# Kernel tuning notes

Measured on AMD Instinct MI355X. Metric: run time of the kernel, lower is better.

The kernel has to match this reference:

```python
import jax, jax.numpy as jnp
import numpy as np

B, L, D = 2, 2048, 2048
H, KV = 32, 8
HD = D // H          # 64
REP = H // KV        # 4


def setup_inputs() -> dict:
    key = jax.random.key(0)
    ks = jax.random.split(key, 6)
    x = jax.random.normal(ks[0], (B, L, D), dtype=jnp.float32)
    # weights stored [in, out] (transpose of torch Linear weight), scaled for stability
    wq = jax.random.normal(ks[1], (D, H * HD), dtype=jnp.float32) * 0.02
    wk = jax.random.normal(ks[2], (D, KV * HD), dtype=jnp.float32) * 0.02
    wv = jax.random.normal(ks[3], (D, KV * HD), dtype=jnp.float32) * 0.02
    wo = jax.random.normal(ks[4], (H * HD, D), dtype=jnp.float32) * 0.02
    # RoPE frequencies: freqs_cis = exp(i * pos * theta), theta_j = 10000^{-2j/HD}
    inv_freq = 1.0 / (10000.0 ** (jnp.arange(0, HD, 2, dtype=jnp.float32) / HD))  # [HD/2]
    angles = jnp.arange(L, dtype=jnp.float32)[:, None] * inv_freq[None, :]        # [L, HD/2]
    freqs_cos = jnp.cos(angles)
    freqs_sin = jnp.sin(angles)
    # additive causal mask [L, L] (prefill from start_pos=0)
    mask = jnp.where(jnp.tril(jnp.ones((L, L), dtype=bool)), 0.0, -jnp.inf).astype(jnp.float32)
    return {"x": x, "start_pos": 0, "freqs_cos": freqs_cos, "freqs_sin": freqs_sin,
            "mask": mask, "wq": wq, "wk": wk, "wv": wv, "wo": wo}


def _apply_rope(t, cos, sin):
    # t: [B, L, h, HD]; cos/sin: [L, HD/2] -> broadcast [1, L, 1, HD/2]
    tp = t.reshape(*t.shape[:-1], HD // 2, 2)
    a, b = tp[..., 0], tp[..., 1]
    c = cos[None, :, None, :]
    s = sin[None, :, None, :]
    ra = a * c - b * s
    rb = a * s + b * c
    return jnp.stack([ra, rb], axis=-1).reshape(t.shape)


def reference(x, start_pos, freqs_cos, freqs_sin, mask, wq, wk, wv, wo):
    xq = jnp.einsum('bld,de->ble', x, wq).reshape(B, L, H, HD)
    xk = jnp.einsum('bld,de->ble', x, wk).reshape(B, L, KV, HD)
    xv = jnp.einsum('bld,de->ble', x, wv).reshape(B, L, KV, HD)
    xq = _apply_rope(xq, freqs_cos, freqs_sin)
    xk = _apply_rope(xk, freqs_cos, freqs_sin)
    # (cache write of xk/xv is a dead side effect in the torch module; omitted)
    # GQA: query head (g*REP + r) attends to kv head g  == repeat_interleave semantics
    q = xq.transpose(0, 2, 1, 3).reshape(B, KV, REP, L, HD)  # [B,KV,REP,L,HD]
    k = xk.transpose(0, 2, 1, 3)                              # [B,KV,L,HD]
    v = xv.transpose(0, 2, 1, 3)
    scale = 1.0 / jnp.sqrt(jnp.float32(HD))
    scores = jnp.einsum('bgrld,bgmd->bgrlm', q, k) * scale + mask  # [B,KV,REP,L,L]
    attn = jax.nn.softmax(scores, axis=-1)
    out = jnp.einsum('bgrlm,bgmd->bgrld', attn, v)            # [B,KV,REP,L,HD]
    out = out.reshape(B, H, L, HD).transpose(0, 2, 1, 3).reshape(B, L, H * HD)
    return jnp.einsum('ble,ed->bld', out, wo)
```

## Files before the change

### kernel.cpp

```cpp
#include <hip/hip_runtime.h>
#include <hip/hip_bf16.h>
#include <math.h>

typedef __bf16 bf16_t;
typedef __bf16 bf16x8 __attribute__((ext_vector_type(8)));
typedef __bf16 bf16x4 __attribute__((ext_vector_type(4)));
typedef __bf16 bf16x2 __attribute__((ext_vector_type(2)));
typedef float  f32x4  __attribute__((ext_vector_type(4)));
typedef int    i32x4  __attribute__((ext_vector_type(4)));

#define B_  2
#define L_  2048
#define D_  2048
#define H_  32
#define KV_ 8
#define HD_ 64

static __device__ __forceinline__ void gload_lds16(const bf16_t* g, void* l)
{
    __builtin_amdgcn_global_load_lds(
        (const __attribute__((address_space(1))) void*)g,
        (__attribute__((address_space(3))) void*)l, 16, 0, 0);
}

static __device__ __forceinline__ int packbf(float a, float b)
{
    bf16x2 t; t[0] = (bf16_t)a; t[1] = (bf16_t)b;
    return __builtin_bit_cast(int, t);
}

static __device__ __forceinline__ void pl32(int& a, int& b)
{
    asm("v_permlane32_swap_b32 %0, %1" : "+v"(a), "+v"(b));
}
static __device__ __forceinline__ void pl16(int& a, int& b)
{
    asm("v_permlane16_swap_b32 %0, %1" : "+v"(a), "+v"(b));
}

#define WAITV8() asm volatile("s_waitcnt vmcnt(8)" ::: "memory")
#define WAITV4() asm volatile("s_waitcnt vmcnt(4)" ::: "memory")
#define WAITV2() asm volatile("s_waitcnt vmcnt(2)" ::: "memory")
#define WAITV0() asm volatile("s_waitcnt vmcnt(0)" ::: "memory")
#define WAITL0() asm volatile("s_waitcnt lgkmcnt(0)" ::: "memory")

__global__ void cast_f32_bf16(const float4* __restrict__ in,
                              bf16x4* __restrict__ out, int n4)
{
    const int i = blockIdx.x * 256 + threadIdx.x;
    if (i >= n4) return;
    const float4 v = in[i];
    bf16x4 o;
    o[0] = (bf16_t)v.x; o[1] = (bf16_t)v.y; o[2] = (bf16_t)v.z; o[3] = (bf16_t)v.w;
    out[i] = o;
}

template <typename InT>
__global__ void transpose_cast(const InT* __restrict__ in, bf16_t* __restrict__ out,
                               int R, int C)
{
    __shared__ bf16_t tile[32][33];
    const int bx = blockIdx.x * 32, by = blockIdx.y * 32;
    in  += (size_t)blockIdx.z * R * C;
    out += (size_t)blockIdx.z * R * C;
    const int tx = threadIdx.x, ty = threadIdx.y;
#pragma unroll
    for (int i = ty; i < 32; i += 8)
        tile[i][tx] = (bf16_t)(float)in[(size_t)(by + i) * C + bx + tx];
    __syncthreads();
#pragma unroll
    for (int i = ty; i < 32; i += 8)
        out[(size_t)(bx + i) * R + by + tx] = tile[tx][i];
}

#define FRAG(base, row, kk) \
    (*(const bf16x8*)((base) + (size_t)(row) * 128 + ((((kk) * 4 + quad) ^ sw8) << 4)))

#define STG_A(kt, h, buf) do {                                                        \
    gload_lds16(Ag + (size_t)((h) * 128)      * 2048 + (size_t)(kt) * 64,             \
                sdst + (buf) * 32768 + (h) * 16384);                                  \
    gload_lds16(Ag + (size_t)((h) * 128 + 64) * 2048 + (size_t)(kt) * 64,             \
                sdst + (buf) * 32768 + (h) * 16384 + 8192);                           \
} while (0)

#define STG_B(kt, h, buf) do {                                                        \
    gload_lds16(Bg + (size_t)((h) * 128)      * 2048 + (size_t)(kt) * 64,             \
                sdst + 65536 + (buf) * 32768 + (h) * 16384);                          \
    gload_lds16(Bg + (size_t)((h) * 128 + 64) * 2048 + (size_t)(kt) * 64,             \
                sdst + 65536 + (buf) * 32768 + (h) * 16384 + 8192);                   \
} while (0)

#define PHASE_SET(AB, BB, STG1, STG2, STG3, STG4, VM4)                                \
  {                                        \
    _Pragma("unroll") for (int m = 0; m < 4; m++) {                                   \
        Afr[m][0] = FRAG(AB, arow + m * 16, 0);                                       \
        Afr[m][1] = FRAG(AB, arow + m * 16, 1); }                                     \
    _Pragma("unroll") for (int n = 0; n < 2; n++) {                                   \
        B01[n][0] = FRAG(BB, brow + n * 16, 0);                                       \
        B01[n][1] = FRAG(BB, brow + n * 16, 1); }                                     \
    STG1;                                                                             \
    asm volatile("s_waitcnt lgkmcnt(8)" ::: "memory");                                \
    __builtin_amdgcn_s_barrier();                                                     \
    WAITL0();                                                                         \
    __builtin_amdgcn_s_setprio(1);                                                    \
    _Pragma("unroll") for (int m = 0; m < 4; m++)                                     \
      _Pragma("unroll") for (int n = 0; n < 2; n++)                                   \
        _Pragma("unroll") for (int kk = 0; kk < 2; kk++)                              \
          acc[m][n] = __builtin_amdgcn_mfma_f32_16x16x32_bf16(                        \
              Afr[m][kk], B01[n][kk], acc[m][n], 0, 0, 0);                            \
    __builtin_amdgcn_s_setprio(0);                                                    \
    __builtin_amdgcn_s_barrier();                                                     \
  }                                                                                   \
  {                                                 \
    _Pragma("unroll") for (int n = 0; n < 2; n++) {                                   \
        B23[n][0] = FRAG(BB, brow + (n + 2) * 16, 0);                                 \
        B23[n][1] = FRAG(BB, brow + (n + 2) * 16, 1); }                               \
    STG2;                                                                             \
    __builtin_amdgcn_s_barrier();                                                     \
    WAITL0();                                                                         \
    __builtin_amdgcn_s_setprio(1);                                                    \
    _Pragma("unroll") for (int m = 0; m < 4; m++)                                     \
      _Pragma("unroll") for (int n = 0; n < 2; n++)                                   \
        _Pragma("unroll") for (int kk = 0; kk < 2; kk++)                              \
          acc[m][n + 2] = __builtin_amdgcn_mfma_f32_16x16x32_bf16(                    \
              Afr[m][kk], B23[n][kk], acc[m][n + 2], 0, 0, 0);                        \
    __builtin_amdgcn_s_setprio(0);                                                    \
    __builtin_amdgcn_s_barrier();                                                     \
  }                                                                                   \
  {                                                 \
    _Pragma("unroll") for (int m = 0; m < 4; m++) {                                   \
        Afr[m][0] = FRAG(AB, arow + (m + 4) * 16, 0);                                 \
        Afr[m][1] = FRAG(AB, arow + (m + 4) * 16, 1); }                               \
    STG3;                                                                             \
    __builtin_amdgcn_s_barrier();                                                     \
    WAITL0();                                                                         \
    __builtin_amdgcn_s_setprio(1);                                                    \
    _Pragma("unroll") for (int m = 0; m < 4; m++)                                     \
      _Pragma("unroll") for (int n = 0; n < 2; n++)                                   \
        _Pragma("unroll") for (int kk = 0; kk < 2; kk++)                              \
          acc[m + 4][n + 2] = __builtin_amdgcn_mfma_f32_16x16x32_bf16(                \
              Afr[m][kk], B23[n][kk], acc[m + 4][n + 2], 0, 0, 0);                    \
    __builtin_amdgcn_s_setprio(0);                                                    \
    __builtin_amdgcn_s_barrier();                                                     \
  }                                                                                   \
  {                                        \
    STG4;                                                                             \
    VM4;                                                                              \
    __builtin_amdgcn_s_barrier();                                                     \
    __builtin_amdgcn_s_setprio(1);                                                    \
    _Pragma("unroll") for (int m = 0; m < 4; m++)                                     \
      _Pragma("unroll") for (int n = 0; n < 2; n++)                                   \
        _Pragma("unroll") for (int kk = 0; kk < 2; kk++)                              \
          acc[m + 4][n] = __builtin_amdgcn_mfma_f32_16x16x32_bf16(                    \
              Afr[m][kk], B01[n][kk], acc[m + 4][n], 0, 0, 0);                        \
    __builtin_amdgcn_s_setprio(0);                                                    \
    __builtin_amdgcn_s_barrier();                                                     \
  }

__global__ __launch_bounds__(512, 2) void gemm_qkv(
    const bf16_t* __restrict__ A,
    const bf16_t* __restrict__ BT,
    bf16_t* __restrict__ Qb, bf16_t* __restrict__ Kb, bf16_t* __restrict__ Vb)
{
    extern __shared__ __attribute__((aligned(16))) char DLDS[];
    constexpr int NITER = 2048 / 64 / 2;

    const int tid  = threadIdx.x;
    const int wave = tid >> 6;
    const int lane = tid & 63;
    const int quad = lane >> 4;
    const int l16  = lane & 15;
    const int wr   = wave >> 2;
    const int wc   = wave & 3;
    const int m0   = blockIdx.y * 256;
    const int n0   = blockIdx.x * 256;

    const int srow  = tid >> 3;
    const int swcol = ((tid & 7) ^ (srow & 7)) * 8;
    const bf16_t* Ag = A  + (size_t)(m0 + srow) * 2048 + swcol;
    const bf16_t* Bg = BT + (size_t)(n0 + srow) * 2048 + swcol;
    char* sdst = DLDS + tid * 16;

    const char* AB0 = DLDS;
    const char* AB1 = DLDS + 32768;
    const char* BB0 = DLDS + 65536;
    const char* BB1 = DLDS + 98304;
    const int sw8  = l16 & 7;
    const int arow = wr * 128 + l16;
    const int brow = wc * 64 + l16;

    f32x4 acc[8][4];
    const f32x4 zf = {0.f, 0.f, 0.f, 0.f};
#pragma unroll
    for (int i = 0; i < 8; i++)
#pragma unroll
        for (int j = 0; j < 4; j++) acc[i][j] = zf;

    bf16x8 Afr[4][2], B01[2][2], B23[2][2];

    STG_B(0, 0, 0); STG_B(0, 1, 0); STG_A(0, 0, 0); STG_A(0, 1, 0);
    STG_B(1, 0, 1); STG_B(1, 1, 1);
    WAITV4();
    __builtin_amdgcn_s_barrier();

    for (int i = 0; i < NITER; ++i) {
        const int t1 = 2 * i + 1;
        const int t2 = 2 * i + 2;
        const int t3 = 2 * i + 3;
        const bool more = (i + 1 < NITER);

        PHASE_SET(AB0, BB0,
                  STG_A(t1, 0, 1),
                  STG_A(t1, 1, 1),
                  if (more) STG_B(t2, 0, 0),
                  if (more) STG_B(t2, 1, 0),
                  if (more) { WAITV4(); } else { WAITV0(); })
        PHASE_SET(AB1, BB1,
                  if (more) STG_A(t2, 0, 0),
                  if (more) STG_A(t2, 1, 0),
                  if (more) STG_B(t3, 0, 1),
                  if (more) STG_B(t3, 1, 1),
                  WAITV4())
    }

    bf16_t* Cb; int ldc, coff; float cs = 1.f;
    if (n0 < 2048)      { Cb = Qb; ldc = 2048; coff = 0; }
    else if (n0 < 2560) { Cb = Kb; ldc = 512;  coff = 2048;
                          cs = 0.18033688011112042f; }
    else                { Cb = Vb; ldc = 512;  coff = 2560; }

#pragma unroll
    for (int mt = 0; mt < 8; mt++)
#pragma unroll
        for (int nt = 0; nt < 4; nt++)
#pragma unroll
            for (int r = 0; r < 4; r++) {
                const int row = m0 + wr * 128 + mt * 16 + quad * 4 + r;
                const int col = n0 + wc * 64 + nt * 16 + l16 - coff;
                Cb[(size_t)row * ldc + col] = (bf16_t)(acc[mt][nt][r] * cs);
            }
}

#undef FRAG
#undef STG_A
#undef STG_B
#undef PHASE_SET

#define OFRAG(base, row, kk) \
    (*(const bf16x8*)((base) + (size_t)(row) * 128 + ((((kk) * 4 + quad) ^ sw8) << 4)))

#define OSTG_A(kt, h, buf) do {                                                       \
    gload_lds16(Ag + (size_t)((h) * 128)      * 2048 + (size_t)(kt) * 64,             \
                adst + (buf) * 32768 + (h) * 16384);                                  \
    gload_lds16(Ag + (size_t)((h) * 128 + 64) * 2048 + (size_t)(kt) * 64,             \
                adst + (buf) * 32768 + (h) * 16384 + 8192);                           \
} while (0)

#define OSTG_B(kt, buf) do {                                                          \
    gload_lds16(Bg + (size_t)(kt) * 64,                       bdst + (buf) * 16384);  \
    gload_lds16(Bg + (size_t)64 * 2048 + (size_t)(kt) * 64,   bdst + (buf) * 16384 + 8192); \
} while (0)

#define OTILE(AB, BB, SA, SB, VMW)                                                    \
  {                                             \
    _Pragma("unroll") for (int m = 0; m < 4; m++) {                                   \
        Afr[m][0] = OFRAG(AB, arow + m * 16, 0);                                      \
        Afr[m][1] = OFRAG(AB, arow + m * 16, 1); }                                    \
    _Pragma("unroll") for (int n = 0; n < 2; n++) {                                   \
        Bfr[n][0] = OFRAG(BB, brow + n * 16, 0);                                      \
        Bfr[n][1] = OFRAG(BB, brow + n * 16, 1); }                                    \
    SA;                                                                               \
    asm volatile("s_waitcnt lgkmcnt(8)" ::: "memory");                                \
    __builtin_amdgcn_s_barrier();                                                     \
    WAITL0();                                                                         \
    __builtin_amdgcn_s_setprio(1);                                                    \
    _Pragma("unroll") for (int m = 0; m < 4; m++)                                     \
      _Pragma("unroll") for (int n = 0; n < 2; n++)                                   \
        _Pragma("unroll") for (int kk = 0; kk < 2; kk++)                              \
          acc[m][n] = __builtin_amdgcn_mfma_f32_16x16x32_bf16(                        \
              Afr[m][kk], Bfr[n][kk], acc[m][n], 0, 0, 0);                            \
    __builtin_amdgcn_s_setprio(0);                                                    \
    __builtin_amdgcn_s_barrier();                                                     \
  }                                                                                   \
  {                                \
    _Pragma("unroll") for (int m = 0; m < 4; m++) {                                   \
        Afr[m][0] = OFRAG(AB, arow + (m + 4) * 16, 0);                                \
        Afr[m][1] = OFRAG(AB, arow + (m + 4) * 16, 1); }                              \
    SB;                                                                               \
    VMW;                                                                              \
    __builtin_amdgcn_s_barrier();                                                     \
    WAITL0();                                                                         \
    __builtin_amdgcn_s_setprio(1);                                                    \
    _Pragma("unroll") for (int m = 0; m < 4; m++)                                     \
      _Pragma("unroll") for (int n = 0; n < 2; n++)                                   \
        _Pragma("unroll") for (int kk = 0; kk < 2; kk++)                              \
          acc[m + 4][n] = __builtin_amdgcn_mfma_f32_16x16x32_bf16(                    \
              Afr[m][kk], Bfr[n][kk], acc[m + 4][n], 0, 0, 0);                        \
    __builtin_amdgcn_s_setprio(0);                                                    \
    __builtin_amdgcn_s_barrier();                                                     \
  }

__global__ __launch_bounds__(512, 2) void gemm_out(
    const bf16_t* __restrict__ A,
    const bf16_t* __restrict__ BT,
    float* __restrict__ C)
{
    extern __shared__ __attribute__((aligned(16))) char DLDS[];
    constexpr int NITER = 2048 / 64 / 2;

    const int tid  = threadIdx.x;
    const int wave = tid >> 6;
    const int lane = tid & 63;
    const int quad = lane >> 4;
    const int l16  = lane & 15;
    const int wr   = wave >> 2;
    const int wc   = wave & 3;

    const int id   = blockIdx.x;
    const int w    = id >> 3;
    const int m0   = ((id & 7) * 2 + (w & 1)) * 256;
    const int n0   = (w >> 1) * 128;

    const int srow  = tid >> 3;
    const int swcol = ((tid & 7) ^ (srow & 7)) * 8;
    const bf16_t* Ag = A  + (size_t)(m0 + srow) * 2048 + swcol;
    const bf16_t* Bg = BT + (size_t)(n0 + srow) * 2048 + swcol;
    char* adst = DLDS + tid * 16;
    char* bdst = DLDS + 65536 + tid * 16;

    const char* AB0 = DLDS;
    const char* AB1 = DLDS + 32768;
    const char* BB0 = DLDS + 65536;
    const char* BB1 = DLDS + 81920;
    const int sw8  = l16 & 7;
    const int arow = wr * 128 + l16;
    const int brow = wc * 32 + l16;

    f32x4 acc[8][2];
    const f32x4 zf = {0.f, 0.f, 0.f, 0.f};
#pragma unroll
    for (int i = 0; i < 8; i++)
#pragma unroll
        for (int j = 0; j < 2; j++) acc[i][j] = zf;

    bf16x8 Afr[4][2], Bfr[2][2];

    OSTG_B(0, 0); OSTG_A(0, 0, 0); OSTG_A(0, 1, 0); OSTG_B(1, 1);
    WAITV2();
    __builtin_amdgcn_s_barrier();

    for (int i = 0; i < NITER; ++i) {
        const int v  = 2 * i + 1;
        const int t2 = 2 * i + 2;
        const int t3 = 2 * i + 3;
        const bool more = (i + 1 < NITER);

        OTILE(AB0, BB0,
              { OSTG_A(v, 0, 1); OSTG_A(v, 1, 1); },
              { if (more) OSTG_B(t2, 0); },
              if (more) { WAITV2(); } else { WAITV0(); })
        OTILE(AB1, BB1,
              { if (more) { OSTG_A(t2, 0, 0); OSTG_A(t2, 1, 0); } },
              { if (more) OSTG_B(t3, 1); },
              if (more) { WAITV2(); } else { WAITV0(); })
    }

#pragma unroll
    for (int mt = 0; mt < 8; mt++)
#pragma unroll
        for (int nt = 0; nt < 2; nt++)
#pragma unroll
            for (int r = 0; r < 4; r++) {
                const int row = m0 + wr * 128 + mt * 16 + quad * 4 + r;
                const int col = n0 + wc * 32 + nt * 16 + l16;
                C[(size_t)row * 2048 + col] = acc[mt][nt][r];
            }
}

#undef OFRAG
#undef OSTG_A
#undef OSTG_B
#undef OTILE

__global__ void rope_k(bf16_t* __restrict__ T, const float* __restrict__ fc,
                       const float* __restrict__ fs, int nheads, int total8)
{
    const int idx = blockIdx.x * 256 + threadIdx.x;
    if (idx >= total8) return;
    const int g  = idx & 7;
    const int t  = idx >> 3;
    const int h  = t % nheads;
    const int bl = t / nheads;
    const int l  = bl & (L_ - 1);
    const float4 c4 = *(const float4*)(fc + l * 32 + g * 4);
    const float4 s4 = *(const float4*)(fs + l * 32 + g * 4);
    const size_t off = ((size_t)bl * nheads + h) * 64 + g * 8;
    const bf16x8 v = *(const bf16x8*)(T + off);
    const float cc[4] = {c4.x, c4.y, c4.z, c4.w};
    const float ss[4] = {s4.x, s4.y, s4.z, s4.w};
    bf16x8 o;
#pragma unroll
    for (int p = 0; p < 4; p++) {
        const float a  = (float)v[2 * p];
        const float b2 = (float)v[2 * p + 1];
        o[2 * p]     = (bf16_t)(a * cc[p] - b2 * ss[p]);
        o[2 * p + 1] = (bf16_t)(a * ss[p] + b2 * cc[p]);
    }
    *(bf16x8*)(T + off) = o;
}

__global__ __launch_bounds__(256, 2) void attn_k(
    const bf16_t* __restrict__ Q,
    const bf16_t* __restrict__ Kc,
    const bf16_t* __restrict__ VT,
    bf16_t* __restrict__ Ob)
{
    __shared__ __attribute__((aligned(16))) char LDS[65536];
    float* OL = (float*)LDS;
    float* LR = (float*)(LDS + 17408);

    const int tid  = threadIdx.x;
    const int wave = tid >> 6;
    const int lane = tid & 63;
    const int quad = lane >> 4;
    const int l16  = lane & 15;

    const int id   = blockIdx.y * 16 + blockIdx.x;
    const int c    = (id >> 3) & 15;
    const int bh   = (id & 7) * 8 + (id >> 7);
    const int bb   = bh >> 5;
    const int h    = bh & 31;
    const int kvh  = h >> 2;
    const size_t bbL = (size_t)bb * L_;

    const int schunk = ((lane & 3) ^ ((lane >> 3) & 3)) * 8;
    const int sw16   = ((l16 >> 1) & 3) * 16;

    const bf16_t* Kg = Kc + bbL * (KV_ * HD_) + kvh * HD_;
    const bf16_t* Vg = VT + (size_t)(bb * KV_ + kvh) * HD_ * L_;
    const bf16_t* KgL = Kg + (size_t)(wave * 32 + (lane >> 2)) * (KV_ * HD_) + schunk;
    const bf16_t* VgL = Vg + (size_t)(lane >> 2) * L_ + wave * 32 + schunk;
    char* kdst0 = (char*)LDS + wave * 2048 + (lane << 4);
    char* vdst0 = (char*)LDS + 16384 + wave * 4096 + (lane << 4);

    const f32x4 zf = {0.f, 0.f, 0.f, 0.f};

    for (int half = 0; half < 2; ++half) {
        const int j     = half ? c : 31 - c;
        const int qbase = j * 64;
        const int nkt   = (j + 2) >> 1;

        bf16x8 qf[4][2];
#pragma unroll
        for (int qt = 0; qt < 4; qt++) {
            const bf16_t* qrow = Q + ((bbL + qbase + qt * 16 + l16) * H_ + h) * HD_;
            qf[qt][0] = *(const bf16x8*)(qrow + quad * 8);
            qf[qt][1] = *(const bf16x8*)(qrow + 32 + quad * 8);
        }

        f32x4 acc[4][4];
#pragma unroll
        for (int mt = 0; mt < 4; mt++)
#pragma unroll
            for (int qt = 0; qt < 4; qt++) acc[mt][qt] = zf;
        float lacc[4] = {0.f, 0.f, 0.f, 0.f};

        {
            const int ktb = 0;
#pragma unroll
            for (int cc = 0; cc < 2; cc++)
#pragma unroll
                for (int sub = 0; sub < 2; sub++)
                    gload_lds16(KgL + (size_t)(ktb + sub * 16) * (KV_ * HD_) + cc * 32,
                                kdst0 + cc * 8192 + sub * 1024);
#pragma unroll
            for (int sub = 0; sub < 4; sub++)
                gload_lds16(VgL + (size_t)(sub * 16) * L_ + ktb,
                            vdst0 + sub * 1024);
        }

        for (int kt = 0; kt < nkt; kt++) {
            if (kt + 1 < nkt) {
                WAITL0();
                const int d = ((kt + 1) & 1) * 32768;
                const int ktb = (kt + 1) * 128;
#pragma unroll
                for (int cc = 0; cc < 2; cc++)
#pragma unroll
                    for (int sub = 0; sub < 2; sub++)
                        gload_lds16(KgL + (size_t)(ktb + sub * 16) * (KV_ * HD_) + cc * 32,
                                    kdst0 + d + cc * 8192 + sub * 1024);
#pragma unroll
                for (int sub = 0; sub < 4; sub++)
                    gload_lds16(VgL + (size_t)(sub * 16) * L_ + ktb,
                                vdst0 + d + sub * 1024);
                WAITV8();
            } else {
                WAITV0();
            }

            const char* Kld = LDS + (kt & 1) * 32768;
            const char* Vld = Kld + 16384;

            bf16x8 kf[2][2];
#pragma unroll
            for (int t = 0; t < 2; t++)
#pragma unroll
                for (int cc = 0; cc < 2; cc++)
                    kf[t][cc] = *(const bf16x8*)(Kld + cc * 8192 +
                        (wave * 32 + t * 16 + l16) * 64 + ((quad * 16) ^ sw16));

            bf16x8 vf[4];
#pragma unroll
            for (int mt = 0; mt < 4; mt++)
                vf[mt] = *(const bf16x8*)(Vld + wave * 4096 +
                    (mt * 16 + l16) * 64 + ((quad * 16) ^ sw16));

            f32x4 st[2][4];
            __builtin_amdgcn_s_setprio(1);
#pragma unroll
            for (int t = 0; t < 2; t++)
#pragma unroll
                for (int qt = 0; qt < 4; qt++) {
                    f32x4 s = __builtin_amdgcn_mfma_f32_16x16x32_bf16(
                        kf[t][0], qf[qt][0], zf, 0, 0, 0);
                    st[t][qt] = __builtin_amdgcn_mfma_f32_16x16x32_bf16(
                        kf[t][1], qf[qt][1], s, 0, 0, 0);
                }
            __builtin_amdgcn_s_setprio(0);

            if (kt == nkt - 1) {
                const int kq = kt * 128 + wave * 32 + quad * 4 - qbase - l16;
#pragma unroll
                for (int t = 0; t < 2; t++)
#pragma unroll
                    for (int qt = 0; qt < 4; qt++)
#pragma unroll
                        for (int r = 0; r < 4; r++)
                            st[t][qt][r] = (kq + t * 16 - qt * 16 + r <= 0)
                                         ? st[t][qt][r] : -__builtin_inff();
            }

            int pk[2][4][2];
#pragma unroll
            for (int t = 0; t < 2; t++)
#pragma unroll
                for (int qt = 0; qt < 4; qt++) {
                    const float e0 = __builtin_amdgcn_exp2f(st[t][qt][0]);
                    const float e1 = __builtin_amdgcn_exp2f(st[t][qt][1]);
                    const float e2 = __builtin_amdgcn_exp2f(st[t][qt][2]);
                    const float e3 = __builtin_amdgcn_exp2f(st[t][qt][3]);
                    lacc[qt] += (e0 + e1) + (e2 + e3);
                    pk[t][qt][0] = packbf(e0, e1);
                    pk[t][qt][1] = packbf(e2, e3);
                }

#pragma unroll
            for (int qt = 0; qt < 4; qt++) {
                int a0 = pk[0][qt][0], b0 = pk[1][qt][0];
                pl32(a0, b0); pl16(a0, b0);
                int a1 = pk[0][qt][1], b1 = pk[1][qt][1];
                pl32(a1, b1); pl16(a1, b1);
                i32x4 bi;
                bi[0] = a0; bi[1] = a1; bi[2] = b0; bi[3] = b1;
                const bf16x8 pb = __builtin_bit_cast(bf16x8, bi);
                __builtin_amdgcn_s_setprio(1);
#pragma unroll
                for (int mt = 0; mt < 4; mt++)
                    acc[mt][qt] = __builtin_amdgcn_mfma_f32_16x16x32_bf16(
                        vf[mt], pb, acc[mt][qt], 0, 0, 0);
                __builtin_amdgcn_s_setprio(0);
            }
        }

        float lw[4];
#pragma unroll
        for (int qt = 0; qt < 4; qt++) {
            float v = lacc[qt];
            v += __shfl_xor(v, 16);
            v += __shfl_xor(v, 32);
            lw[qt] = v;
        }

        __syncthreads();

        if (quad == 0)
#pragma unroll
            for (int qt = 0; qt < 4; qt++)
                LR[(wave * 4 + qt) * 16 + l16] = lw[qt];

#pragma unroll
        for (int p = 0; p < 4; p++) {
#pragma unroll
            for (int qt = 0; qt < 4; qt++) {
                if (((qt - wave) & 3) == p) {
#pragma unroll
                    for (int mt = 0; mt < 4; mt++) {
                        float* a = OL + (qt * 16 + l16) * 68 + mt * 16 + quad * 4;
                        if (p == 0) *(f32x4*)a = acc[mt][qt];
                        else        *(f32x4*)a = *(f32x4*)a + acc[mt][qt];
                    }
                }
            }
            __syncthreads();
        }

        const float ls = LR[(0 * 4 + wave) * 16 + l16] + LR[(1 * 4 + wave) * 16 + l16]
                       + LR[(2 * 4 + wave) * 16 + l16] + LR[(3 * 4 + wave) * 16 + l16];
        const float inv = 1.f / ls;
        bf16_t* orow = Ob + ((bbL + qbase + wave * 16 + l16) * H_ + h) * HD_;
#pragma unroll
        for (int j2 = 0; j2 < 4; j2++) {
            const f32x4 v = *(const f32x4*)(OL + (wave * 16 + l16) * 68 + quad * 16 + j2 * 4);
            bf16x4 o;
#pragma unroll
            for (int i = 0; i < 4; i++) o[i] = (bf16_t)(v[i] * inv);
            *(bf16x4*)(orow + quad * 16 + j2 * 4) = o;
        }
        __syncthreads();
    }
}

extern "C" void kernel_launch(void* const* d_in, const int* in_sizes, int n_in,
                              void* d_out, int out_size, void* d_ws, size_t ws_size,
                              hipStream_t stream)
{
    (void)in_sizes; (void)n_in; (void)out_size; (void)ws_size;
    const float* xf = (const float*)d_in[0];
    const float* fc = (const float*)d_in[2];
    const float* fs = (const float*)d_in[3];
    const float* wq = (const float*)d_in[5];
    const float* wk = (const float*)d_in[6];
    const float* wv = (const float*)d_in[7];
    const float* wo = (const float*)d_in[8];
    float* out = (float*)d_out;

    char* ws = (char*)d_ws;
    bf16_t* xb   = (bf16_t*)(ws);
    bf16_t* Qb   = (bf16_t*)(ws + (16ull << 20));
    bf16_t* Kb   = (bf16_t*)(ws + (32ull << 20));
    bf16_t* Vb   = (bf16_t*)(ws + (36ull << 20));
    bf16_t* VTb  = (bf16_t*)(ws + (40ull << 20));
    bf16_t* Oa   = (bf16_t*)(ws + (44ull << 20));
    bf16_t* Wqkv = (bf16_t*)(ws + (60ull << 20));
    bf16_t* WoT  = (bf16_t*)(ws + (72ull << 20));

    cast_f32_bf16<<<8192, 256, 0, stream>>>((const float4*)xf, (bf16x4*)xb,
                                            B_ * L_ * D_ / 4);

    const dim3 tb(32, 8);
    transpose_cast<float><<<dim3(64, 64, 1), tb, 0, stream>>>(wq, Wqkv, 2048, 2048);
    transpose_cast<float><<<dim3(16, 64, 1), tb, 0, stream>>>(wk, Wqkv + 2048ull * 2048, 2048, 512);
    transpose_cast<float><<<dim3(16, 64, 1), tb, 0, stream>>>(wv, Wqkv + 2560ull * 2048, 2048, 512);
    transpose_cast<float><<<dim3(64, 64, 1), tb, 0, stream>>>(wo, WoT, 2048, 2048);

    gemm_qkv<<<dim3(12, 16), 512, 131072, stream>>>(xb, Wqkv, Qb, Kb, Vb);

    rope_k<<<4096, 256, 0, stream>>>(Qb, fc, fs, 32, B_ * L_ * 32 * 8);
    rope_k<<<1024, 256, 0, stream>>>(Kb, fc, fs, 8, B_ * L_ * 8 * 8);

    transpose_cast<bf16_t><<<dim3(16, 64, 2), tb, 0, stream>>>(Vb, VTb, 2048, 512);

    attn_k<<<dim3(16, 64), 256, 0, stream>>>(Qb, Kb, VTb, Oa);

    gemm_out<<<dim3(256), 512, 98304, stream>>>(Oa, WoT, out);
}
```

Before: 308.0 us.

## Fuse RoPE into QKV GEMM epilogue and single-buffer attention K/V LDS

```diff
diff --git a/kernel.cpp b/kernel.cpp
--- a/kernel.cpp
+++ b/kernel.cpp
@@ -38,7 +38,6 @@
     asm("v_permlane16_swap_b32 %0, %1" : "+v"(a), "+v"(b));
 }
 
-#define WAITV8() asm volatile("s_waitcnt vmcnt(8)" ::: "memory")
 #define WAITV4() asm volatile("s_waitcnt vmcnt(4)" ::: "memory")
 #define WAITV2() asm volatile("s_waitcnt vmcnt(2)" ::: "memory")
 #define WAITV0() asm volatile("s_waitcnt vmcnt(0)" ::: "memory")
@@ -160,7 +159,8 @@
 __global__ __launch_bounds__(512, 2) void gemm_qkv(
     const bf16_t* __restrict__ A,
     const bf16_t* __restrict__ BT,
-    bf16_t* __restrict__ Qb, bf16_t* __restrict__ Kb, bf16_t* __restrict__ Vb)
+    bf16_t* __restrict__ Qb, bf16_t* __restrict__ Kb, bf16_t* __restrict__ Vb,
+    const float* __restrict__ fc, const float* __restrict__ fs)
 {
     extern __shared__ __attribute__((aligned(16))) char DLDS[];
     constexpr int NITER = 2048 / 64 / 2;
@@ -228,6 +228,7 @@
     else if (n0 < 2560) { Cb = Kb; ldc = 512;  coff = 2048;
                           cs = 0.18033688011112042f; }
     else                { Cb = Vb; ldc = 512;  coff = 2560; }
+    const bool dorope = (n0 < 2560);
 
 #pragma unroll
     for (int mt = 0; mt < 8; mt++)
@@ -237,7 +238,16 @@
             for (int r = 0; r < 4; r++) {
                 const int row = m0 + wr * 128 + mt * 16 + quad * 4 + r;
                 const int col = n0 + wc * 64 + nt * 16 + l16 - coff;
-                Cb[(size_t)row * ldc + col] = (bf16_t)(acc[mt][nt][r] * cs);
+                float v = acc[mt][nt][r];
+                if (dorope) {
+                    const float p = __shfl_xor(v, 1);
+                    const int l  = row & (L_ - 1);
+                    const int ri = nt * 8 + (l16 >> 1);
+                    const float cR = fc[l * 32 + ri];
+                    const float sR = fs[l * 32 + ri];
+                    v = (l16 & 1) ? (p * sR + v * cR) : (v * cR - p * sR);
+                }
+                Cb[(size_t)row * ldc + col] = (bf16_t)(v * cs);
             }
 }
 
@@ -382,40 +392,13 @@
 #undef OSTG_B
 #undef OTILE
 
-__global__ void rope_k(bf16_t* __restrict__ T, const float* __restrict__ fc,
-                       const float* __restrict__ fs, int nheads, int total8)
-{
-    const int idx = blockIdx.x * 256 + threadIdx.x;
-    if (idx >= total8) return;
-    const int g  = idx & 7;
-    const int t  = idx >> 3;
-    const int h  = t % nheads;
-    const int bl = t / nheads;
-    const int l  = bl & (L_ - 1);
-    const float4 c4 = *(const float4*)(fc + l * 32 + g * 4);
-    const float4 s4 = *(const float4*)(fs + l * 32 + g * 4);
-    const size_t off = ((size_t)bl * nheads + h) * 64 + g * 8;
-    const bf16x8 v = *(const bf16x8*)(T + off);
-    const float cc[4] = {c4.x, c4.y, c4.z, c4.w};
-    const float ss[4] = {s4.x, s4.y, s4.z, s4.w};
-    bf16x8 o;
-#pragma unroll
-    for (int p = 0; p < 4; p++) {
-        const float a  = (float)v[2 * p];
-        const float b2 = (float)v[2 * p + 1];
-        o[2 * p]     = (bf16_t)(a * cc[p] - b2 * ss[p]);
-        o[2 * p + 1] = (bf16_t)(a * ss[p] + b2 * cc[p]);
-    }
-    *(bf16x8*)(T + off) = o;
-}
-
 __global__ __launch_bounds__(256, 2) void attn_k(
     const bf16_t* __restrict__ Q,
     const bf16_t* __restrict__ Kc,
     const bf16_t* __restrict__ VT,
     bf16_t* __restrict__ Ob)
 {
-    __shared__ __attribute__((aligned(16))) char LDS[65536];
+    __shared__ __attribute__((aligned(16))) char LDS[32768];
     float* OL = (float*)LDS;
     float* LR = (float*)(LDS + 17408);
 
@@ -465,42 +448,21 @@
             for (int qt = 0; qt < 4; qt++) acc[mt][qt] = zf;
         float lacc[4] = {0.f, 0.f, 0.f, 0.f};
 
-        {
-            const int ktb = 0;
-#pragma unroll
-            for (int cc = 0; cc < 2; cc++)
-#pragma unroll
-                for (int sub = 0; sub < 2; sub++)
-                    gload_lds16(KgL + (size_t)(ktb + sub * 16) * (KV_ * HD_) + cc * 32,
-                                kdst0 + cc * 8192 + sub * 1024);
-#pragma unroll
-            for (int sub = 0; sub < 4; sub++)
-                gload_lds16(VgL + (size_t)(sub * 16) * L_ + ktb,
-                            vdst0 + sub * 1024);
-        }
+#pragma unroll
+        for (int cc = 0; cc < 2; cc++)
+#pragma unroll
+            for (int sub = 0; sub < 2; sub++)
+                gload_lds16(KgL + (size_t)(sub * 16) * (KV_ * HD_) + cc * 32,
+                            kdst0 + cc * 8192 + sub * 1024);
+#pragma unroll
+        for (int sub = 0; sub < 4; sub++)
+            gload_lds16(VgL + (size_t)(sub * 16) * L_, vdst0 + sub * 1024);
 
         for (int kt = 0; kt < nkt; kt++) {
-            if (kt + 1 < nkt) {
-                WAITL0();
-                const int d = ((kt + 1) & 1) * 32768;
-                const int ktb = (kt + 1) * 128;
-#pragma unroll
-                for (int cc = 0; cc < 2; cc++)
-#pragma unroll
-                    for (int sub = 0; sub < 2; sub++)
-                        gload_lds16(KgL + (size_t)(ktb + sub * 16) * (KV_ * HD_) + cc * 32,
-                                    kdst0 + d + cc * 8192 + sub * 1024);
-#pragma unroll
-                for (int sub = 0; sub < 4; sub++)
-                    gload_lds16(VgL + (size_t)(sub * 16) * L_ + ktb,
-                                vdst0 + d + sub * 1024);
-                WAITV8();
-            } else {
-                WAITV0();
-            }
-
-            const char* Kld = LDS + (kt & 1) * 32768;
-            const char* Vld = Kld + 16384;
+            WAITV0();
+
+            const char* Kld = LDS;
+            const char* Vld = LDS + 16384;
 
             bf16x8 kf[2][2];
 #pragma unroll
@@ -515,6 +477,22 @@
             for (int mt = 0; mt < 4; mt++)
                 vf[mt] = *(const bf16x8*)(Vld + wave * 4096 +
                     (mt * 16 + l16) * 64 + ((quad * 16) ^ sw16));
+
+            WAITL0();
+
+            if (kt + 1 < nkt) {
+                const int ktb = (kt + 1) * 128;
+#pragma unroll
+                for (int cc = 0; cc < 2; cc++)
+#pragma unroll
+                    for (int sub = 0; sub < 2; sub++)
+                        gload_lds16(KgL + (size_t)(ktb + sub * 16) * (KV_ * HD_) + cc * 32,
+                                    kdst0 + cc * 8192 + sub * 1024);
+#pragma unroll
+                for (int sub = 0; sub < 4; sub++)
+                    gload_lds16(VgL + (size_t)(sub * 16) * L_ + ktb,
+                                vdst0 + sub * 1024);
+            }
 
             f32x4 st[2][4];
             __builtin_amdgcn_s_setprio(1);
@@ -654,10 +632,7 @@
     transpose_cast<float><<<dim3(16, 64, 1), tb, 0, stream>>>(wv, Wqkv + 2560ull * 2048, 2048, 512);
     transpose_cast<float><<<dim3(64, 64, 1), tb, 0, stream>>>(wo, WoT, 2048, 2048);
 
-    gemm_qkv<<<dim3(12, 16), 512, 131072, stream>>>(xb, Wqkv, Qb, Kb, Vb);
-
-    rope_k<<<4096, 256, 0, stream>>>(Qb, fc, fs, 32, B_ * L_ * 32 * 8);
-    rope_k<<<1024, 256, 0, stream>>>(Kb, fc, fs, 8, B_ * L_ * 8 * 8);
+    gemm_qkv<<<dim3(12, 16), 512, 131072, stream>>>(xb, Wqkv, Qb, Kb, Vb, fc, fs);
 
     transpose_cast<bf16_t><<<dim3(16, 64, 2), tb, 0, stream>>>(Vb, VTb, 2048, 512);
 
```

New measurement: 324.3 us. +5.3%, slower.
